# Kernel optimization log

Hardware: AMD Instinct MI355X
Metric: run time of the kernel (lower is better)

The kernel has to match this reference:

```python
import jax, jax.numpy as jnp
import numpy as np

# Circuit per wire i: |0> -RX(x_i)-> -RY(theta_i)-> measure PauliZ.
# Because every gate is single-qubit on its own wire, the state stays a
# product state and <Z_i> has the closed form cos(theta_i) * cos(x_i)
# (derived from |a|^2-|b|^2 of RY(th)RX(x)|0>). This computes the exact
# same math as the torchquantum state-vector loop, fully fused/batched.

N_QUBITS = 16
BATCH, SEQ = 128, 8192

def setup_inputs() -> dict:
    key = jax.random.key(0)
    kx, kt, kw, kb = jax.random.split(key, 4)
    x = jax.random.normal(kx, (BATCH, SEQ, N_QUBITS), dtype=jnp.float32)
    # trainable RY angles (tq.RY has_params init) and Linear(n_qubits, 1)
    theta = jax.random.normal(kt, (N_QUBITS,), dtype=jnp.float32)
    bound = 1.0 / np.sqrt(N_QUBITS)
    w = jax.random.uniform(kw, (1, N_QUBITS), dtype=jnp.float32, minval=-bound, maxval=bound)
    b = jax.random.uniform(kb, (1,), dtype=jnp.float32, minval=-bound, maxval=bound)
    return {"x": x, "theta": theta, "w": w, "b": b}

def reference(x, theta, w, b):
    # <Z_i> = cos(theta_i) * cos(x_i)  per token, all wires at once
    z = jnp.cos(x) * jnp.cos(theta)            # [B, S, Q]
    out = jnp.einsum('bsq,oq->bso', z, w) + b  # [B, S, 1]
    return out
```

## Files before the change

### kernel.cpp

```cpp
#include <hip/hip_runtime.h>

#define NQ 16

__global__ __launch_bounds__(256) void qfc_kernel(
    const float* __restrict__ x,
    const float* __restrict__ theta,
    const float* __restrict__ w,
    const float* __restrict__ bias,
    float* __restrict__ out,
    int ntok)
{
    int t = blockIdx.x * blockDim.x + threadIdx.x;
    if (t >= ntok) return;

    float ct[NQ];
#pragma unroll
    for (int q = 0; q < NQ; ++q) ct[q] = __cosf(theta[q]) * w[q];

    const float4* xv = reinterpret_cast<const float4*>(x) + (size_t)t * (NQ / 4);
    float acc = bias[0];
#pragma unroll
    for (int m = 0; m < 4; ++m) {
        float4 v = xv[m];
        acc += __cosf(v.x) * ct[4 * m + 0];
        acc += __cosf(v.y) * ct[4 * m + 1];
        acc += __cosf(v.z) * ct[4 * m + 2];
        acc += __cosf(v.w) * ct[4 * m + 3];
    }
    out[t] = acc;
}

extern "C" void kernel_launch(void* const* d_in, const int* in_sizes, int n_in,
                              void* d_out, int out_size, void* d_ws, size_t ws_size,
                              hipStream_t stream) {
    const float* x     = (const float*)d_in[0];
    const float* theta = (const float*)d_in[1];
    const float* w     = (const float*)d_in[2];
    const float* bias  = (const float*)d_in[3];
    float* out = (float*)d_out;

    int ntok = out_size;
    int block = 256;
    int grid = (ntok + block - 1) / block;
    qfc_kernel<<<grid, block, 0, stream>>>(x, theta, w, bias, out, ntok);
}
```

Measured before the change: 16.20 us.

## Precompute cos(theta)*w in prep kernel and process two tokens per thread

Adds a tiny prep kernel that computes cos(theta)*w and the bias into workspace, so the main kernel no longer evaluates 16 cosines per thread. The main kernel now handles two tokens per thread, issuing eight float4 loads up front and writing a float2 output, which raises memory-level parallelism per thread. The cost is an extra kernel launch and a dependency between the two launches, and out_size must be even.

Measured after the change: 21.31 us. +31.6%, slower.

```diff
diff --git a/kernel.cpp b/kernel.cpp
--- a/kernel.cpp
+++ b/kernel.cpp
@@ -2,32 +2,53 @@
 
 #define NQ 16
 
+__global__ void qfc_prep(const float* __restrict__ theta,
+                         const float* __restrict__ w,
+                         const float* __restrict__ bias,
+                         float* __restrict__ ws)
+{
+    int q = threadIdx.x;
+    if (q < NQ) ws[q] = __cosf(theta[q]) * w[q];
+    if (q == NQ) ws[NQ] = bias[0];
+}
+
 __global__ __launch_bounds__(256) void qfc_kernel(
     const float* __restrict__ x,
-    const float* __restrict__ theta,
-    const float* __restrict__ w,
-    const float* __restrict__ bias,
+    const float* __restrict__ ws,
     float* __restrict__ out,
-    int ntok)
+    int ntok2)
 {
     int t = blockIdx.x * blockDim.x + threadIdx.x;
-    if (t >= ntok) return;
+    if (t >= ntok2) return;
 
     float ct[NQ];
 #pragma unroll
-    for (int q = 0; q < NQ; ++q) ct[q] = __cosf(theta[q]) * w[q];
+    for (int q = 0; q < NQ; ++q) ct[q] = ws[q];
+    float bias = ws[NQ];
 
-    const float4* xv = reinterpret_cast<const float4*>(x) + (size_t)t * (NQ / 4);
-    float acc = bias[0];
+    const float4* xv = reinterpret_cast<const float4*>(x) + (size_t)t * 8;
+
+    float4 v[8];
+#pragma unroll
+    for (int m = 0; m < 8; ++m) v[m] = xv[m];
+
+    float acc0 = bias, acc1 = bias;
 #pragma unroll
     for (int m = 0; m < 4; ++m) {
-        float4 v = xv[m];
-        acc += __cosf(v.x) * ct[4 * m + 0];
-        acc += __cosf(v.y) * ct[4 * m + 1];
-        acc += __cosf(v.z) * ct[4 * m + 2];
-        acc += __cosf(v.w) * ct[4 * m + 3];
+        acc0 += __cosf(v[m].x) * ct[4 * m + 0];
+        acc0 += __cosf(v[m].y) * ct[4 * m + 1];
+        acc0 += __cosf(v[m].z) * ct[4 * m + 2];
+        acc0 += __cosf(v[m].w) * ct[4 * m + 3];
     }
-    out[t] = acc;
+#pragma unroll
+    for (int m = 0; m < 4; ++m) {
+        acc1 += __cosf(v[4 + m].x) * ct[4 * m + 0];
+        acc1 += __cosf(v[4 + m].y) * ct[4 * m + 1];
+        acc1 += __cosf(v[4 + m].z) * ct[4 * m + 2];
+        acc1 += __cosf(v[4 + m].w) * ct[4 * m + 3];
+    }
+
+    reinterpret_cast<float2*>(out)[t] = make_float2(acc0, acc1);
 }
 
 extern "C" void kernel_launch(void* const* d_in, const int* in_sizes, int n_in,
@@ -38,9 +59,12 @@
     const float* w     = (const float*)d_in[2];
     const float* bias  = (const float*)d_in[3];
     float* out = (float*)d_out;
+    float* ws  = (float*)d_ws;
 
-    int ntok = out_size;
+    qfc_prep<<<1, 64, 0, stream>>>(theta, w, bias, ws);
+
+    int ntok2 = out_size / 2;
     int block = 256;
-    int grid = (ntok + block - 1) / block;
-    qfc_kernel<<<grid, block, 0, stream>>>(x, theta, w, bias, out, ntok);
+    int grid = (ntok2 + block - 1) / block;
+    qfc_kernel<<<grid, block, 0, stream>>>(x, ws, out, ntok2);
 }
```

## Split each token across four lanes with coalesced float4 loads and shuffle reduction

Applied to the files above, without the earlier changes.

Reassigns work so four adjacent lanes share one token, each loading one float4 of its 16 inputs. A wave's loads become fully contiguous, and each lane keeps only four precomputed cos(theta)*w coefficients instead of sixteen. Partial sums are combined with two xor shuffles, and one lane in four writes the result. Each wave now covers 256 tokens with four batched loads per group. The bounds check is gone, so the kernel assumes the token count is a multiple of 1024.

After: 17.14 us. +5.8%, slower.

```diff
diff --git a/kernel.cpp b/kernel.cpp
--- a/kernel.cpp
+++ b/kernel.cpp
@@ -1,33 +1,44 @@
 #include <hip/hip_runtime.h>
 
-#define NQ 16
-
-__global__ __launch_bounds__(256) void qfc_kernel(
+__global__ __launch_bounds__(256, 8) void qfc_kernel(
     const float* __restrict__ x,
     const float* __restrict__ theta,
     const float* __restrict__ w,
     const float* __restrict__ bias,
-    float* __restrict__ out,
-    int ntok)
+    float* __restrict__ out)
 {
-    int t = blockIdx.x * blockDim.x + threadIdx.x;
-    if (t >= ntok) return;
+    const int lane = threadIdx.x & 63;
+    const long wave = (long)blockIdx.x * 4 + (threadIdx.x >> 6);
 
-    float ct[NQ];
+    const int q4 = lane & 3;
+    float4 th = reinterpret_cast<const float4*>(theta)[q4];
+    float4 ww = reinterpret_cast<const float4*>(w)[q4];
+    float c0 = __cosf(th.x) * ww.x;
+    float c1 = __cosf(th.y) * ww.y;
+    float c2 = __cosf(th.z) * ww.z;
+    float c3 = __cosf(th.w) * ww.w;
+    float bb = bias[0];
+
+    const float4* xv = reinterpret_cast<const float4*>(x) + wave * 1024 + lane;
+    float* outw = out + wave * 256;
+
+    const int j = lane >> 2;
+    const bool writer = (q4 == 0);
+
 #pragma unroll
-    for (int q = 0; q < NQ; ++q) ct[q] = __cosf(theta[q]) * w[q];
-
-    const float4* xv = reinterpret_cast<const float4*>(x) + (size_t)t * (NQ / 4);
-    float acc = bias[0];
+    for (int g = 0; g < 4; ++g) {
+        float4 v[4];
 #pragma unroll
-    for (int m = 0; m < 4; ++m) {
-        float4 v = xv[m];
-        acc += __cosf(v.x) * ct[4 * m + 0];
-        acc += __cosf(v.y) * ct[4 * m + 1];
-        acc += __cosf(v.z) * ct[4 * m + 2];
-        acc += __cosf(v.w) * ct[4 * m + 3];
+        for (int r = 0; r < 4; ++r) v[r] = xv[(g * 4 + r) * 64];
+#pragma unroll
+        for (int r = 0; r < 4; ++r) {
+            float s = __cosf(v[r].x) * c0 + __cosf(v[r].y) * c1
+                    + __cosf(v[r].z) * c2 + __cosf(v[r].w) * c3;
+            s += __shfl_xor(s, 1);
+            s += __shfl_xor(s, 2);
+            if (writer) outw[(g * 4 + r) * 16 + j] = s + bb;
+        }
     }
-    out[t] = acc;
 }
 
 extern "C" void kernel_launch(void* const* d_in, const int* in_sizes, int n_in,
@@ -39,8 +50,7 @@
     const float* bias  = (const float*)d_in[3];
     float* out = (float*)d_out;
 
-    int ntok = out_size;
-    int block = 256;
-    int grid = (ntok + block - 1) / block;
-    qfc_kernel<<<grid, block, 0, stream>>>(x, theta, w, bias, out, ntok);
+    int waves = out_size / 256;
+    int grid = waves / 4;
+    qfc_kernel<<<grid, 256, 0, stream>>>(x, theta, w, bias, out);
 }
```
